# Optimization experiments

Hardware: AMD Instinct MI355X
Metric: run time of the kernel (lower is better)

Reference implementation:

```python
import jax, jax.numpy as jnp
import numpy as np

VTH = 0.5      # sp.vth_init
TAU = 0.25     # sp.tau_mem


def setup_inputs() -> dict:
    key = jax.random.key(0)
    x = jax.random.normal(key, (64, 2048, 256), dtype=jnp.float32)  # [B, C, T]
    return {"x": x}


def reference(x):
    """LIF integrate-fire-reset over the last (time) axis.

    Per step (STBP-style lif_update):
        u_t   = tau * u_{t-1} * (1 - spike_{t-1}) + x_t   # leaky integrate + reset
        s_t   = (u_t > vth)                                # fire
    Initial u and spike are zeros (matches out[..., max(step-1,0)] at step 0).
    """
    x_t = jnp.moveaxis(x, -1, 0)  # [T, B, C] for scan over time
    u0 = jnp.zeros(x.shape[:-1], dtype=x.dtype)
    s0 = jnp.zeros(x.shape[:-1], dtype=x.dtype)

    def step(carry, xt):
        u, s_prev = carry
        u = TAU * u * (1.0 - s_prev) + xt
        s = (u > VTH).astype(x.dtype)
        return (u, s), s

    _, spikes = jax.lax.scan(step, (u0, s0), x_t)  # spikes: [T, B, C]
    return jnp.moveaxis(spikes, 0, -1)  # [B, C, T]
```

## Files before the change

### kernel.cpp

```cpp
#include <hip/hip_runtime.h>


#define T_LEN 256
#define CT 32
#define NCH (T_LEN / CT)
#define RPB 256
#define XS_STRIDE 36

#define TAU 0.25f
#define VTH 0.5f

__global__ __launch_bounds__(RPB, 4)
void lif_kernel(const float* __restrict__ x, float* __restrict__ out) {
    __shared__ __align__(16) float xs[RPB * XS_STRIDE];
    __shared__ unsigned int smask[RPB];

    const int tid = threadIdx.x;
    const long rbase = (long)blockIdx.x * RPB;

    const float4* __restrict__ x4 = reinterpret_cast<const float4*>(x);
    float4* __restrict__ o4 = reinterpret_cast<float4*>(out);

    float u = 0.0f;
    bool sprev = false;

    for (int k = 0; k < NCH; ++k) {
        const int t0q = k * (CT / 4);

        #pragma unroll
        for (int i = 0; i < 8; ++i) {
            int flat = i * RPB + tid;
            int row  = flat >> 3;
            int g    = flat & 7;
            float4 v = x4[(rbase + row) * (T_LEN / 4) + t0q + g];
            *reinterpret_cast<float4*>(&xs[row * XS_STRIDE + 4 * g]) = v;
        }
        __syncthreads();

        float4 v[8];
        #pragma unroll
        for (int i = 0; i < 8; ++i)
            v[i] = *reinterpret_cast<const float4*>(&xs[tid * XS_STRIDE + 4 * i]);

        unsigned int m = 0;
        #pragma unroll
        for (int i = 0; i < 8; ++i) {
            float e0 = v[i].x, e1 = v[i].y, e2 = v[i].z, e3 = v[i].w;
            {
                float um = sprev ? 0.0f : __fmul_rn(TAU, u);
                u = __fadd_rn(um, e0);
                sprev = u > VTH;
                m |= (sprev ? 1u : 0u) << (i * 4 + 0);
            }
            {
                float um = sprev ? 0.0f : __fmul_rn(TAU, u);
                u = __fadd_rn(um, e1);
                sprev = u > VTH;
                m |= (sprev ? 1u : 0u) << (i * 4 + 1);
            }
            {
                float um = sprev ? 0.0f : __fmul_rn(TAU, u);
                u = __fadd_rn(um, e2);
                sprev = u > VTH;
                m |= (sprev ? 1u : 0u) << (i * 4 + 2);
            }
            {
                float um = sprev ? 0.0f : __fmul_rn(TAU, u);
                u = __fadd_rn(um, e3);
                sprev = u > VTH;
                m |= (sprev ? 1u : 0u) << (i * 4 + 3);
            }
        }
        smask[tid] = m;
        __syncthreads();

        #pragma unroll
        for (int i = 0; i < 8; ++i) {
            int flat = i * RPB + tid;
            int row  = flat >> 3;
            int g    = flat & 7;
            unsigned int mr = smask[row];
            int toff = 4 * g;
            float4 o;
            o.x = ((mr >> (toff + 0)) & 1u) ? 1.0f : 0.0f;
            o.y = ((mr >> (toff + 1)) & 1u) ? 1.0f : 0.0f;
            o.z = ((mr >> (toff + 2)) & 1u) ? 1.0f : 0.0f;
            o.w = ((mr >> (toff + 3)) & 1u) ? 1.0f : 0.0f;
            o4[(rbase + row) * (T_LEN / 4) + t0q + g] = o;
        }
    }
}

extern "C" void kernel_launch(void* const* d_in, const int* in_sizes, int n_in,
                              void* d_out, int out_size, void* d_ws, size_t ws_size,
                              hipStream_t stream) {
    const float* x = (const float*)d_in[0];
    float* out = (float*)d_out;
    const int total = in_sizes[0];
    const int nrows = total / T_LEN;
    const int blocks = nrows / RPB;
    lif_kernel<<<blocks, RPB, 0, stream>>>(x, out);
}
```

Measured before the change: 46.50 us.

## Prefetch next time chunk into registers, double-buffer LDS, shuffle spike masks

Global loads for the next 32-step time chunk are issued into registers right after the barrier, so they overlap the sequential LIF recurrence on the current chunk. LDS is double-buffered, which drops one barrier per chunk. Spike masks now reach the store lanes through wavefront shuffles instead of shared memory, and outputs are written with nontemporal stores. In exchange, register pressure rises and launch bounds are lowered to 2 blocks per SM, which reduces occupancy.

```diff
diff --git a/kernel.cpp b/kernel.cpp
--- a/kernel.cpp
+++ b/kernel.cpp
@@ -2,91 +2,86 @@
 
 
 #define T_LEN 256
-#define CT 32
-#define NCH (T_LEN / CT)
+#define TQ 64
+#define NCH 8
 #define RPB 256
 #define XS_STRIDE 36
 
 #define TAU 0.25f
 #define VTH 0.5f
 
-__global__ __launch_bounds__(RPB, 4)
+typedef float f32x4 __attribute__((ext_vector_type(4)));
+
+__global__ __launch_bounds__(RPB, 2)
 void lif_kernel(const float* __restrict__ x, float* __restrict__ out) {
-    __shared__ __align__(16) float xs[RPB * XS_STRIDE];
-    __shared__ unsigned int smask[RPB];
+    __shared__ __align__(16) float xs[2][RPB * XS_STRIDE];
 
-    const int tid = threadIdx.x;
+    const int tid  = threadIdx.x;
+    const int lane = tid & 63;
+    const int wv   = tid >> 6;
     const long rbase = (long)blockIdx.x * RPB;
 
     const float4* __restrict__ x4 = reinterpret_cast<const float4*>(x);
-    float4* __restrict__ o4 = reinterpret_cast<float4*>(out);
+    float* __restrict__ outp = out;
+
+    const int qs = tid & 7;
+    const int rs = tid >> 3;
+
+    float4 p[8];
+    #pragma unroll
+    for (int i = 0; i < 8; ++i)
+        p[i] = x4[(rbase + rs + i * 32) * TQ + qs];
 
     float u = 0.0f;
     bool sprev = false;
 
+    #pragma unroll
     for (int k = 0; k < NCH; ++k) {
-        const int t0q = k * (CT / 4);
+        float* buf = xs[k & 1];
 
         #pragma unroll
-        for (int i = 0; i < 8; ++i) {
-            int flat = i * RPB + tid;
-            int row  = flat >> 3;
-            int g    = flat & 7;
-            float4 v = x4[(rbase + row) * (T_LEN / 4) + t0q + g];
-            *reinterpret_cast<float4*>(&xs[row * XS_STRIDE + 4 * g]) = v;
+        for (int i = 0; i < 8; ++i)
+            *reinterpret_cast<float4*>(&buf[(rs + i * 32) * XS_STRIDE + 4 * qs]) = p[i];
+
+        asm volatile("s_waitcnt lgkmcnt(0)" ::: "memory");
+        __builtin_amdgcn_s_barrier();
+
+        if (k + 1 < NCH) {
+            #pragma unroll
+            for (int i = 0; i < 8; ++i)
+                p[i] = x4[(rbase + rs + i * 32) * TQ + (k + 1) * 8 + qs];
         }
-        __syncthreads();
 
         float4 v[8];
         #pragma unroll
         for (int i = 0; i < 8; ++i)
-            v[i] = *reinterpret_cast<const float4*>(&xs[tid * XS_STRIDE + 4 * i]);
+            v[i] = *reinterpret_cast<const float4*>(&buf[tid * XS_STRIDE + 4 * i]);
 
         unsigned int m = 0;
         #pragma unroll
         for (int i = 0; i < 8; ++i) {
-            float e0 = v[i].x, e1 = v[i].y, e2 = v[i].z, e3 = v[i].w;
-            {
+            float e[4] = { v[i].x, v[i].y, v[i].z, v[i].w };
+            #pragma unroll
+            for (int j = 0; j < 4; ++j) {
                 float um = sprev ? 0.0f : __fmul_rn(TAU, u);
-                u = __fadd_rn(um, e0);
+                u = __fadd_rn(um, e[j]);
                 sprev = u > VTH;
-                m |= (sprev ? 1u : 0u) << (i * 4 + 0);
-            }
-            {
-                float um = sprev ? 0.0f : __fmul_rn(TAU, u);
-                u = __fadd_rn(um, e1);
-                sprev = u > VTH;
-                m |= (sprev ? 1u : 0u) << (i * 4 + 1);
-            }
-            {
-                float um = sprev ? 0.0f : __fmul_rn(TAU, u);
-                u = __fadd_rn(um, e2);
-                sprev = u > VTH;
-                m |= (sprev ? 1u : 0u) << (i * 4 + 2);
-            }
-            {
-                float um = sprev ? 0.0f : __fmul_rn(TAU, u);
-                u = __fadd_rn(um, e3);
-                sprev = u > VTH;
-                m |= (sprev ? 1u : 0u) << (i * 4 + 3);
+                m |= (sprev ? 1u : 0u) << (i * 4 + j);
             }
         }
-        smask[tid] = m;
-        __syncthreads();
 
         #pragma unroll
         for (int i = 0; i < 8; ++i) {
-            int flat = i * RPB + tid;
-            int row  = flat >> 3;
-            int g    = flat & 7;
-            unsigned int mr = smask[row];
-            int toff = 4 * g;
-            float4 o;
-            o.x = ((mr >> (toff + 0)) & 1u) ? 1.0f : 0.0f;
-            o.y = ((mr >> (toff + 1)) & 1u) ? 1.0f : 0.0f;
-            o.z = ((mr >> (toff + 2)) & 1u) ? 1.0f : 0.0f;
-            o.w = ((mr >> (toff + 3)) & 1u) ? 1.0f : 0.0f;
-            o4[(rbase + row) * (T_LEN / 4) + t0q + g] = o;
+            int rowl = i * 8 + (lane >> 3);
+            unsigned int mr = (unsigned int)__shfl((int)m, rowl, 64);
+            int toff = 4 * (lane & 7);
+            f32x4 o;
+            o[0] = ((mr >> (toff + 0)) & 1u) ? 1.0f : 0.0f;
+            o[1] = ((mr >> (toff + 1)) & 1u) ? 1.0f : 0.0f;
+            o[2] = ((mr >> (toff + 2)) & 1u) ? 1.0f : 0.0f;
+            o[3] = ((mr >> (toff + 3)) & 1u) ? 1.0f : 0.0f;
+            long gq = (rbase + wv * 64 + rowl) * (long)TQ + k * 8 + (lane & 7);
+            __builtin_nontemporal_store(o, reinterpret_cast<f32x4*>(outp) + gq);
         }
     }
 }
```

After: 44.81 us, median of 2. 3.6% less time.
